# Optimization experiments

Hardware: AMD Instinct MI355X
Metric: run time of the kernel (lower is better)

## Reference

```python
import jax, jax.numpy as jnp
import numpy as np

B, S, D = 4, 2048, 1024
H, DK, DV, DFF = 16, 64, 64, 4096
EPS = 1e-5


def layer_norm(x, g, b):
    mu = jnp.mean(x, axis=-1, keepdims=True)
    var = jnp.mean((x - mu) ** 2, axis=-1, keepdims=True)
    return (x - mu) * jax.lax.rsqrt(var + EPS) * g + b


def setup_inputs() -> dict:
    key = jax.random.key(0)
    ks = jax.random.split(key, 12)
    s = lambda fan_in: 1.0 / np.sqrt(fan_in)
    return {
        "x": jax.random.normal(ks[0], (B, S, D), dtype=jnp.float32),
        # per-head projections stacked: [H, D, DK/DV] (x @ W layout)
        "Wq": jax.random.normal(ks[1], (H, D, DK), dtype=jnp.float32) * s(D),
        "Wk": jax.random.normal(ks[2], (H, D, DK), dtype=jnp.float32) * s(D),
        "Wv": jax.random.normal(ks[3], (H, D, DV), dtype=jnp.float32) * s(D),
        "Wo": jax.random.normal(ks[4], (H * DV, D), dtype=jnp.float32) * s(H * DV),
        "ln1_g": jnp.ones((D,), dtype=jnp.float32),
        "ln1_b": jnp.zeros((D,), dtype=jnp.float32),
        "W1": jax.random.normal(ks[5], (D, DFF), dtype=jnp.float32) * s(D),
        "b1": jnp.zeros((DFF,), dtype=jnp.float32),
        "W2": jax.random.normal(ks[6], (DFF, D), dtype=jnp.float32) * s(DFF),
        "b2": jnp.zeros((D,), dtype=jnp.float32),
        "ln2_g": jnp.ones((D,), dtype=jnp.float32),
        "ln2_b": jnp.zeros((D,), dtype=jnp.float32),
    }


def reference(x, Wq, Wk, Wv, Wo, ln1_g, ln1_b, W1, b1, W2, b2, ln2_g, ln2_b):
    # --- multi-head causal self-attention (all heads vectorized) ---
    q = jnp.einsum("bsd,hdk->bhsk", x, Wq)
    k = jnp.einsum("bsd,hdk->bhsk", x, Wk)
    v = jnp.einsum("bsd,hdv->bhsv", x, Wv)
    # NOTE: original scales by 1/sqrt(x.shape[-1]) == 1/sqrt(d_model)
    scale = 1.0 / np.sqrt(D).astype(np.float32)
    scores = jnp.einsum("bhsk,bhtk->bhst", q, k) * scale  # [B,H,S,S]
    causal = jnp.tril(jnp.ones((S, S), dtype=bool))
    scores = jnp.where(causal, scores, -jnp.inf)
    attn = jax.nn.softmax(scores, axis=-1)
    ctx = jnp.einsum("bhst,bhtv->bhsv", attn, v)  # [B,H,S,DV]
    # concat heads (head-major last dim, matches torch.cat order)
    ctx = ctx.transpose(0, 2, 1, 3).reshape(B, S, H * DV)
    attn_out = ctx @ Wo  # [B,S,D]
    # Sublayer 1 (dropout is identity in eval)
    h1 = layer_norm(x + attn_out, ln1_g, ln1_b)
    # --- FFN ---
    ff = jax.nn.relu(h1 @ W1 + b1) @ W2 + b2
    # Sublayer 2
    return layer_norm(h1 + ff, ln2_g, ln2_b)
```

## Files before the change

kernel.cpp:

```cpp
#include <hip/hip_runtime.h>

#define DEV __device__ __forceinline__

using f16x8 = _Float16 __attribute__((ext_vector_type(8)));
using f16x4 = _Float16 __attribute__((ext_vector_type(4)));
using f32x4 = float __attribute__((ext_vector_type(4)));

DEV f32x4 mfma16(f16x8 a, f16x8 b, f32x4 c) {
    return __builtin_amdgcn_mfma_f32_16x16x32_f16(a, b, c, 0, 0, 0);
}

DEV void gload16(const void* g, void* l) {
    __builtin_amdgcn_global_load_lds(
        (const __attribute__((address_space(1))) void*)g,
        (__attribute__((address_space(3))) void*)l, 16, 0, 0);
}

template <int MODE>
__global__ __launch_bounds__(256, 2) void gemm_bt(
    const _Float16* __restrict__ A, const _Float16* __restrict__ Bt,
    int M, int N, int K,
    const float* __restrict__ ep0, const float* __restrict__ ep1,
    void* __restrict__ o0, void* __restrict__ o1, void* __restrict__ o2)
{
    __shared__ __align__(16) _Float16 As[128 * 64];
    __shared__ __align__(16) _Float16 Bs[128 * 64];
    const int tid  = threadIdx.x;
    const int wave = tid >> 6, lane = tid & 63;
    const int l16  = lane & 15, g = lane >> 4;
    const int m0 = blockIdx.x * 128, n0 = blockIdx.y * 128;
    const int wm = (wave >> 1) * 64, wn = (wave & 1) * 64;

    f32x4 acc[4][4] = {};

    for (int kt = 0; kt < K; kt += 64) {
#pragma unroll
        for (int it = 0; it < 4; ++it) {
            const int off  = it * 4096 + tid * 16;
            const int row  = off >> 7;
            const int colb = (off & 127) ^ ((row & 7) << 4);
            gload16(A + (size_t)(m0 + row) * K + kt + (colb >> 1), (char*)As + off);
        }
#pragma unroll
        for (int it = 0; it < 4; ++it) {
            const int off  = it * 4096 + tid * 16;
            const int row  = off >> 7;
            const int colb = (off & 127) ^ ((row & 7) << 4);
            gload16(Bt + (size_t)(n0 + row) * K + kt + (colb >> 1), (char*)Bs + off);
        }
        __syncthreads();
#pragma unroll
        for (int kk = 0; kk < 2; ++kk) {
            f16x8 af[4], bfv[4];
#pragma unroll
            for (int i = 0; i < 4; ++i) {
                const int ar = wm + i * 16 + l16;
                const int cb = ((kk * 32 + g * 8) << 1) ^ ((ar & 7) << 4);
                af[i] = *(const f16x8*)((const char*)As + (ar << 7) + cb);
            }
#pragma unroll
            for (int j = 0; j < 4; ++j) {
                const int br = wn + j * 16 + l16;
                const int cb = ((kk * 32 + g * 8) << 1) ^ ((br & 7) << 4);
                bfv[j] = *(const f16x8*)((const char*)Bs + (br << 7) + cb);
            }
#pragma unroll
            for (int i = 0; i < 4; ++i)
#pragma unroll
                for (int j = 0; j < 4; ++j)
                    acc[i][j] = mfma16(af[i], bfv[j], acc[i][j]);
        }
        __syncthreads();
    }

#pragma unroll
    for (int i = 0; i < 4; ++i) {
#pragma unroll
        for (int j = 0; j < 4; ++j) {
#pragma unroll
            for (int r = 0; r < 4; ++r) {
                const int m = m0 + wm + i * 16 + g * 4 + r;
                const int n = n0 + wn + j * 16 + l16;
                const float val = acc[i][j][r];
                if constexpr (MODE == 0) {
                    const int b = m >> 11, s = m & 2047;
                    const int which = n >> 10, hh = (n >> 6) & 15, dd = n & 63;
                    const size_t bh = (size_t)(b * 16 + hh);
                    if (which == 0) {
                        ((_Float16*)o0)[(bh * 2048 + s) * 64 + dd] =
                            (_Float16)(val * 0.04508422f);
                    } else if (which == 1) {
                        ((_Float16*)o1)[(bh * 2048 + s) * 64 + dd] = (_Float16)val;
                    } else {
                        ((_Float16*)o2)[(bh * 64 + dd) * 2048 + s] = (_Float16)val;
                    }
                } else if constexpr (MODE == 1) {
                    const size_t idx = (size_t)m * N + n;
                    ((float*)o0)[idx] = val + ep0[idx];
                } else if constexpr (MODE == 2) {
                    float v = val + ep0[n];
                    ((_Float16*)o0)[(size_t)m * N + n] = (_Float16)(v > 0.f ? v : 0.f);
                } else {
                    const size_t idx = (size_t)m * N + n;
                    ((float*)o0)[idx] = val + ep0[n] + ep1[idx];
                }
            }
        }
    }
}

DEV void stage_kv(const _Float16* __restrict__ Kh, const _Float16* __restrict__ Vh,
                  int kb0, char* ksb, char* vsb, int tid)
{
#pragma unroll
    for (int it = 0; it < 2; ++it) {
        const int off  = it * 4096 + tid * 16;
        const int row  = off >> 7;
        const int colb = (off & 127) ^ ((row & 7) << 4);
        gload16(Kh + (size_t)(kb0 + row) * 64 + (colb >> 1), ksb + off);
    }
#pragma unroll
    for (int it = 0; it < 2; ++it) {
        const int off  = it * 4096 + tid * 16;
        const int row  = off >> 7;
        const int colb = (off & 127) ^ ((row & 7) << 4);
        gload16(Vh + (size_t)row * 2048 + kb0 + (colb >> 1), vsb + off);
    }
}

__global__ __launch_bounds__(256, 4) void attn_kernel(
    const _Float16* __restrict__ Q, const _Float16* __restrict__ Kb,
    const _Float16* __restrict__ Vt, _Float16* __restrict__ ctx)
{
    __shared__ __align__(16) char smem[40960];
    const int tid = threadIdx.x;
    const int w = tid >> 6, lane = tid & 63;
    const int l16 = lane & 15, g = lane >> 4;
    const int lid = blockIdx.x + (blockIdx.y << 4);
    const int bh  = (lid & 7) * 8 + (lid >> 7);
    const int tA  = (lid >> 3) & 15;
    const int b = bh >> 4, h = bh & 15;

    const _Float16* Kh = Kb + (size_t)bh * 2048 * 64;
    const _Float16* Vh = Vt + (size_t)bh * 64 * 2048;
    const int swl = (l16 & 7) << 4;
    char* prow = smem + 32768 + w * 2048 + l16 * 128;

    for (int half = 0; half < 2; ++half) {
        const int T = half ? (31 - tA) : tA;
        const int qbase = T * 64 + w * 16;
        const int qg = qbase + l16;
        const int nt = T + 1;

        const _Float16* qrow = Q + ((size_t)bh * 2048 + qg) * 64;
        const f16x8 qf0 = *(const f16x8*)(qrow + g * 8);
        const f16x8 qf1 = *(const f16x8*)(qrow + 32 + g * 8);

        f32x4 cacc[4] = {};
        float l_run = 0.f;

        stage_kv(Kh, Vh, 0, smem, smem + 16384, tid);
        if (nt > 1) stage_kv(Kh, Vh, 64, smem + 8192, smem + 24576, tid);

        for (int kt = 0; kt < nt; ++kt) {
            const int bufo = (kt & 1) << 13;
            char* kbuf = smem + bufo;
            char* vbuf = smem + 16384 + bufo;

            if (kt + 1 < nt) asm volatile("s_waitcnt vmcnt(4)" ::: "memory");
            else             asm volatile("s_waitcnt vmcnt(0)" ::: "memory");
            __builtin_amdgcn_s_barrier();
            __builtin_amdgcn_sched_barrier(0);

            f32x4 st[4];
            __builtin_amdgcn_s_setprio(1);
#pragma unroll
            for (int s = 0; s < 4; ++s) {
                const char* kr = kbuf + (16 * s + l16) * 128;
                const f16x8 klo = *(const f16x8*)(kr + ((g * 16) ^ swl));
                const f16x8 khi = *(const f16x8*)(kr + ((64 + g * 16) ^ swl));
                f32x4 a0 = {0.f, 0.f, 0.f, 0.f};
                a0 = mfma16(klo, qf0, a0);
                st[s] = mfma16(khi, qf1, a0);
            }
            __builtin_amdgcn_s_setprio(0);

            if (kt == nt - 1) {
#pragma unroll
                for (int s = 0; s < 4; ++s)
#pragma unroll
                    for (int r = 0; r < 4; ++r) {
                        const int kg = kt * 64 + s * 16 + g * 4 + r;
                        if (kg > qg) st[s][r] = -INFINITY;
                    }
            }

            float tsum = 0.f;
#pragma unroll
            for (int s = 0; s < 4; ++s) {
                f16x4 p;
#pragma unroll
                for (int r = 0; r < 4; ++r) {
                    const float e = __builtin_amdgcn_exp2f(st[s][r]);
                    tsum += e;
                    p[r] = (_Float16)e;
                }
                *(f16x4*)(prow + ((s * 32 + g * 8) ^ swl)) = p;
            }
            tsum += __shfl_xor(tsum, 16);
            tsum += __shfl_xor(tsum, 32);
            l_run += tsum;

            const f16x8 pf0 = *(const f16x8*)(prow + ((g * 16) ^ swl));
            const f16x8 pf1 = *(const f16x8*)(prow + ((64 + g * 16) ^ swl));
            __builtin_amdgcn_s_setprio(1);
#pragma unroll
            for (int jt = 0; jt < 4; ++jt) {
                const char* vr = vbuf + (jt * 16 + l16) * 128;
                const f16x8 vlo = *(const f16x8*)(vr + ((g * 16) ^ swl));
                const f16x8 vhi = *(const f16x8*)(vr + ((64 + g * 16) ^ swl));
                cacc[jt] = mfma16(pf0, vlo, cacc[jt]);
                cacc[jt] = mfma16(pf1, vhi, cacc[jt]);
            }
            __builtin_amdgcn_s_setprio(0);

            __builtin_amdgcn_sched_barrier(0);
            __builtin_amdgcn_s_barrier();
            if (kt + 2 < nt)
                stage_kv(Kh, Vh, (kt + 2) * 64, kbuf, vbuf, tid);
        }

        __builtin_amdgcn_s_barrier();

        const float inv = 1.f / l_run;
        f32x4 il;
#pragma unroll
        for (int r = 0; r < 4; ++r) il[r] = __shfl(inv, g * 4 + r);
#pragma unroll
        for (int jt = 0; jt < 4; ++jt)
#pragma unroll
            for (int r = 0; r < 4; ++r)
                ctx[((size_t)b * 2048 + qbase + g * 4 + r) * 1024 + h * 64 + jt * 16 + l16]
                    = (_Float16)(cacc[jt][r] * il[r]);
    }
}

__global__ __launch_bounds__(256) void ln_kernel(
    const float* __restrict__ in, const float* __restrict__ gam, const float* __restrict__ bet,
    float* __restrict__ out32, _Float16* __restrict__ out16)
{
    const int row = blockIdx.x, tid = threadIdx.x;
    const float4 x = ((const float4*)(in + (size_t)row * 1024))[tid];
    float s  = x.x + x.y + x.z + x.w;
    float s2 = x.x * x.x + x.y * x.y + x.z * x.z + x.w * x.w;
#pragma unroll
    for (int o = 32; o > 0; o >>= 1) {
        s  += __shfl_xor(s, o);
        s2 += __shfl_xor(s2, o);
    }
    __shared__ float red[8];
    if ((tid & 63) == 0) { red[tid >> 6] = s; red[4 + (tid >> 6)] = s2; }
    __syncthreads();
    const float S  = red[0] + red[1] + red[2] + red[3];
    const float S2 = red[4] + red[5] + red[6] + red[7];
    const float mu = S * (1.f / 1024.f);
    const float ir = rsqrtf(S2 * (1.f / 1024.f) - mu * mu + 1e-5f);
    const float4 gv = ((const float4*)gam)[tid];
    const float4 bv = ((const float4*)bet)[tid];
    float4 o;
    o.x = (x.x - mu) * ir * gv.x + bv.x;
    o.y = (x.y - mu) * ir * gv.y + bv.y;
    o.z = (x.z - mu) * ir * gv.z + bv.z;
    o.w = (x.w - mu) * ir * gv.w + bv.w;
    if (out32) ((float4*)(out32 + (size_t)row * 1024))[tid] = o;
    if (out16) {
        f16x4 h;
        h[0] = (_Float16)o.x; h[1] = (_Float16)o.y; h[2] = (_Float16)o.z; h[3] = (_Float16)o.w;
        *(f16x4*)(out16 + (size_t)row * 1024 + tid * 4) = h;
    }
}

__global__ __launch_bounds__(256) void cast_f16(const float* __restrict__ in,
                                                _Float16* __restrict__ out, int n4)
{
    const int i = blockIdx.x * 256 + threadIdx.x;
    if (i < n4) {
        const float4 v = ((const float4*)in)[i];
        f16x4 h;
        h[0] = (_Float16)v.x; h[1] = (_Float16)v.y; h[2] = (_Float16)v.z; h[3] = (_Float16)v.w;
        ((f16x4*)out)[i] = h;
    }
}

__global__ __launch_bounds__(256) void transpose_cast(const float* __restrict__ src,
                                                      _Float16* __restrict__ dst, int K, int N)
{
    __shared__ float tile[64][65];
    const int n0 = blockIdx.x * 64, k0 = blockIdx.y * 64;
    const int tid = threadIdx.x;
#pragma unroll
    for (int it = 0; it < 16; ++it) {
        const int idx = it * 256 + tid;
        const int r = idx >> 6, c = idx & 63;
        tile[r][c] = src[(size_t)(k0 + r) * N + n0 + c];
    }
    __syncthreads();
#pragma unroll
    for (int it = 0; it < 16; ++it) {
        const int idx = it * 256 + tid;
        const int r = idx >> 6, c = idx & 63;
        dst[(size_t)(n0 + r) * K + k0 + c] = (_Float16)tile[c][r];
    }
}

__global__ __launch_bounds__(256) void pack_qkv_w(const float* __restrict__ Wq,
                                                  const float* __restrict__ Wk,
                                                  const float* __restrict__ Wv,
                                                  _Float16* __restrict__ dst)
{
    __shared__ float tile[64][65];
    const int n0 = blockIdx.x * 64, d0 = blockIdx.y * 64;
    const int which = n0 >> 10, hh = (n0 >> 6) & 15;
    const float* W = which == 0 ? Wq : (which == 1 ? Wk : Wv);
    const int tid = threadIdx.x;
#pragma unroll
    for (int it = 0; it < 16; ++it) {
        const int idx = it * 256 + tid;
        const int r = idx >> 6, c = idx & 63;
        tile[r][c] = W[((size_t)hh * 1024 + d0 + r) * 64 + c];
    }
    __syncthreads();
#pragma unroll
    for (int it = 0; it < 16; ++it) {
        const int idx = it * 256 + tid;
        const int r = idx >> 6, c = idx & 63;
        dst[(size_t)(n0 + r) * 1024 + d0 + c] = (_Float16)tile[c][r];
    }
}

extern "C" void kernel_launch(void* const* d_in, const int* in_sizes, int n_in,
                              void* d_out, int out_size, void* d_ws, size_t ws_size,
                              hipStream_t stream)
{
    const float* x    = (const float*)d_in[0];
    const float* Wq   = (const float*)d_in[1];
    const float* Wk   = (const float*)d_in[2];
    const float* Wv   = (const float*)d_in[3];
    const float* Wo   = (const float*)d_in[4];
    const float* ln1g = (const float*)d_in[5];
    const float* ln1b = (const float*)d_in[6];
    const float* W1   = (const float*)d_in[7];
    const float* b1   = (const float*)d_in[8];
    const float* W2   = (const float*)d_in[9];
    const float* b2   = (const float*)d_in[10];
    const float* ln2g = (const float*)d_in[11];
    const float* ln2b = (const float*)d_in[12];
    float* out = (float*)d_out;

    char* ws = (char*)d_ws;
    size_t off = 0;
    auto alloc = [&](size_t bytes) {
        void* p = ws + off;
        off += (bytes + 255) & ~(size_t)255;
        return p;
    };
    _Float16* x_h   = (_Float16*)alloc(8192ULL * 1024 * 2);
    _Float16* wqkv  = (_Float16*)alloc(3072ULL * 1024 * 2);
    _Float16* wo_t  = (_Float16*)alloc(1024ULL * 1024 * 2);
    _Float16* w1_t  = (_Float16*)alloc(4096ULL * 1024 * 2);
    _Float16* w2_t  = (_Float16*)alloc(1024ULL * 4096 * 2);
    _Float16* qbuf  = (_Float16*)alloc(8192ULL * 1024 * 2);
    _Float16* kbuf  = (_Float16*)alloc(8192ULL * 1024 * 2);
    _Float16* vt    = (_Float16*)alloc(8192ULL * 1024 * 2);
    _Float16* ctx   = (_Float16*)alloc(8192ULL * 1024 * 2);
    _Float16* ff1   = qbuf;
    float*    resid = (float*)alloc(8192ULL * 1024 * 4);
    float*    h1f   = (float*)alloc(8192ULL * 1024 * 4);
    _Float16* h1h   = (_Float16*)alloc(8192ULL * 1024 * 2);
    if (off > ws_size) return;

    cast_f16<<<8192, 256, 0, stream>>>(x, x_h, 2097152);
    pack_qkv_w<<<dim3(48, 16), 256, 0, stream>>>(Wq, Wk, Wv, wqkv);
    transpose_cast<<<dim3(16, 16), 256, 0, stream>>>(Wo, wo_t, 1024, 1024);
    transpose_cast<<<dim3(64, 16), 256, 0, stream>>>(W1, w1_t, 1024, 4096);
    transpose_cast<<<dim3(16, 64), 256, 0, stream>>>(W2, w2_t, 4096, 1024);

    gemm_bt<0><<<dim3(64, 24), 256, 0, stream>>>(x_h, wqkv, 8192, 3072, 1024,
                                                 nullptr, nullptr, qbuf, kbuf, vt);
    attn_kernel<<<dim3(16, 64), 256, 0, stream>>>(qbuf, kbuf, vt, ctx);
    gemm_bt<1><<<dim3(64, 8), 256, 0, stream>>>(ctx, wo_t, 8192, 1024, 1024,
                                                x, nullptr, resid, nullptr, nullptr);
    ln_kernel<<<8192, 256, 0, stream>>>(resid, ln1g, ln1b, h1f, h1h);
    gemm_bt<2><<<dim3(64, 32), 256, 0, stream>>>(h1h, w1_t, 8192, 4096, 1024,
                                                 b1, nullptr, ff1, nullptr, nullptr);
    gemm_bt<3><<<dim3(64, 8), 256, 0, stream>>>(ff1, w2_t, 8192, 1024, 4096,
                                                b2, h1f, resid, nullptr, nullptr);
    ln_kernel<<<8192, 256, 0, stream>>>(resid, ln2g, ln2b, out, nullptr);
}
```

Baseline: 365.4 us.

## Store residual streams in fp16 and vectorize weight transpose kernels

```diff
diff --git a/kernel.cpp b/kernel.cpp
--- a/kernel.cpp
+++ b/kernel.cpp
@@ -20,7 +20,7 @@
 __global__ __launch_bounds__(256, 2) void gemm_bt(
     const _Float16* __restrict__ A, const _Float16* __restrict__ Bt,
     int M, int N, int K,
-    const float* __restrict__ ep0, const float* __restrict__ ep1,
+    const float* __restrict__ ep0, const _Float16* __restrict__ eph,
     void* __restrict__ o0, void* __restrict__ o1, void* __restrict__ o2)
 {
     __shared__ __align__(16) _Float16 As[128 * 64];
@@ -96,13 +96,13 @@
                     }
                 } else if constexpr (MODE == 1) {
                     const size_t idx = (size_t)m * N + n;
-                    ((float*)o0)[idx] = val + ep0[idx];
+                    ((_Float16*)o0)[idx] = (_Float16)(val + (float)eph[idx]);
                 } else if constexpr (MODE == 2) {
                     float v = val + ep0[n];
                     ((_Float16*)o0)[(size_t)m * N + n] = (_Float16)(v > 0.f ? v : 0.f);
                 } else {
                     const size_t idx = (size_t)m * N + n;
-                    ((float*)o0)[idx] = val + ep0[n] + ep1[idx];
+                    ((_Float16*)o0)[idx] = (_Float16)(val + ep0[n] + (float)eph[idx]);
                 }
             }
         }
@@ -246,11 +246,13 @@
 }
 
 __global__ __launch_bounds__(256) void ln_kernel(
-    const float* __restrict__ in, const float* __restrict__ gam, const float* __restrict__ bet,
+    const _Float16* __restrict__ in, const float* __restrict__ gam,
+    const float* __restrict__ bet,
     float* __restrict__ out32, _Float16* __restrict__ out16)
 {
     const int row = blockIdx.x, tid = threadIdx.x;
-    const float4 x = ((const float4*)(in + (size_t)row * 1024))[tid];
+    const f16x4 xh = *(const f16x4*)(in + (size_t)row * 1024 + tid * 4);
+    float4 x = {(float)xh[0], (float)xh[1], (float)xh[2], (float)xh[3]};
     float s  = x.x + x.y + x.z + x.w;
     float s2 = x.x * x.x + x.y * x.y + x.z * x.z + x.w * x.w;
 #pragma unroll
@@ -295,21 +297,25 @@
 __global__ __launch_bounds__(256) void transpose_cast(const float* __restrict__ src,
                                                       _Float16* __restrict__ dst, int K, int N)
 {
-    __shared__ float tile[64][65];
+    __shared__ float tile[64][68];
     const int n0 = blockIdx.x * 64, k0 = blockIdx.y * 64;
     const int tid = threadIdx.x;
-#pragma unroll
-    for (int it = 0; it < 16; ++it) {
-        const int idx = it * 256 + tid;
-        const int r = idx >> 6, c = idx & 63;
-        tile[r][c] = src[(size_t)(k0 + r) * N + n0 + c];
+    const int rr = tid >> 4, cc = (tid & 15) * 4;
+#pragma unroll
+    for (int it = 0; it < 4; ++it) {
+        const int r = it * 16 + rr;
+        const float4 v = *(const float4*)&src[(size_t)(k0 + r) * N + n0 + cc];
+        tile[r][cc] = v.x; tile[r][cc + 1] = v.y;
+        tile[r][cc + 2] = v.z; tile[r][cc + 3] = v.w;
     }
     __syncthreads();
 #pragma unroll
-    for (int it = 0; it < 16; ++it) {
-        const int idx = it * 256 + tid;
-        const int r = idx >> 6, c = idx & 63;
-        dst[(size_t)(n0 + r) * K + k0 + c] = (_Float16)tile[c][r];
+    for (int it = 0; it < 4; ++it) {
+        const int n = it * 16 + rr;
+        f16x4 h;
+        h[0] = (_Float16)tile[cc + 0][n]; h[1] = (_Float16)tile[cc + 1][n];
+        h[2] = (_Float16)tile[cc + 2][n]; h[3] = (_Float16)tile[cc + 3][n];
+        *(f16x4*)&dst[(size_t)(n0 + n) * K + k0 + cc] = h;
     }
 }
 
@@ -318,23 +324,27 @@
                                                   const float* __restrict__ Wv,
                                                   _Float16* __restrict__ dst)
 {
-    __shared__ float tile[64][65];
+    __shared__ float tile[64][68];
     const int n0 = blockIdx.x * 64, d0 = blockIdx.y * 64;
     const int which = n0 >> 10, hh = (n0 >> 6) & 15;
     const float* W = which == 0 ? Wq : (which == 1 ? Wk : Wv);
     const int tid = threadIdx.x;
-#pragma unroll
-    for (int it = 0; it < 16; ++it) {
-        const int idx = it * 256 + tid;
-        const int r = idx >> 6, c = idx & 63;
-        tile[r][c] = W[((size_t)hh * 1024 + d0 + r) * 64 + c];
+    const int rr = tid >> 4, cc = (tid & 15) * 4;
+#pragma unroll
+    for (int it = 0; it < 4; ++it) {
+        const int r = it * 16 + rr;
+        const float4 v = *(const float4*)&W[((size_t)hh * 1024 + d0 + r) * 64 + cc];
+        tile[r][cc] = v.x; tile[r][cc + 1] = v.y;
+        tile[r][cc + 2] = v.z; tile[r][cc + 3] = v.w;
     }
     __syncthreads();
 #pragma unroll
-    for (int it = 0; it < 16; ++it) {
-        const int idx = it * 256 + tid;
-        const int r = idx >> 6, c = idx & 63;
-        dst[(size_t)(n0 + r) * 1024 + d0 + c] = (_Float16)tile[c][r];
+    for (int it = 0; it < 4; ++it) {
+        const int kk = it * 16 + rr;
+        f16x4 h;
+        h[0] = (_Float16)tile[cc + 0][kk]; h[1] = (_Float16)tile[cc + 1][kk];
+        h[2] = (_Float16)tile[cc + 2][kk]; h[3] = (_Float16)tile[cc + 3][kk];
+        *(f16x4*)&dst[(size_t)(n0 + kk) * 1024 + d0 + cc] = h;
     }
 }
 
@@ -364,19 +374,18 @@
         off += (bytes + 255) & ~(size_t)255;
         return p;
     };
-    _Float16* x_h   = (_Float16*)alloc(8192ULL * 1024 * 2);
-    _Float16* wqkv  = (_Float16*)alloc(3072ULL * 1024 * 2);
-    _Float16* wo_t  = (_Float16*)alloc(1024ULL * 1024 * 2);
-    _Float16* w1_t  = (_Float16*)alloc(4096ULL * 1024 * 2);
-    _Float16* w2_t  = (_Float16*)alloc(1024ULL * 4096 * 2);
-    _Float16* qbuf  = (_Float16*)alloc(8192ULL * 1024 * 2);
-    _Float16* kbuf  = (_Float16*)alloc(8192ULL * 1024 * 2);
-    _Float16* vt    = (_Float16*)alloc(8192ULL * 1024 * 2);
-    _Float16* ctx   = (_Float16*)alloc(8192ULL * 1024 * 2);
-    _Float16* ff1   = qbuf;
-    float*    resid = (float*)alloc(8192ULL * 1024 * 4);
-    float*    h1f   = (float*)alloc(8192ULL * 1024 * 4);
-    _Float16* h1h   = (_Float16*)alloc(8192ULL * 1024 * 2);
+    _Float16* x_h    = (_Float16*)alloc(8192ULL * 1024 * 2);
+    _Float16* wqkv   = (_Float16*)alloc(3072ULL * 1024 * 2);
+    _Float16* wo_t   = (_Float16*)alloc(1024ULL * 1024 * 2);
+    _Float16* w1_t   = (_Float16*)alloc(4096ULL * 1024 * 2);
+    _Float16* w2_t   = (_Float16*)alloc(1024ULL * 4096 * 2);
+    _Float16* qbuf   = (_Float16*)alloc(8192ULL * 1024 * 2);
+    _Float16* kbuf   = (_Float16*)alloc(8192ULL * 1024 * 2);
+    _Float16* vt     = (_Float16*)alloc(8192ULL * 1024 * 2);
+    _Float16* ctx    = (_Float16*)alloc(8192ULL * 1024 * 2);
+    _Float16* ff1    = qbuf;
+    _Float16* residh = (_Float16*)alloc(8192ULL * 1024 * 2);
+    _Float16* h1h    = (_Float16*)alloc(8192ULL * 1024 * 2);
     if (off > ws_size) return;
 
     cast_f16<<<8192, 256, 0, stream>>>(x, x_h, 2097152);
@@ -389,11 +398,11 @@
                                                  nullptr, nullptr, qbuf, kbuf, vt);
     attn_kernel<<<dim3(16, 64), 256, 0, stream>>>(qbuf, kbuf, vt, ctx);
     gemm_bt<1><<<dim3(64, 8), 256, 0, stream>>>(ctx, wo_t, 8192, 1024, 1024,
-                                                x, nullptr, resid, nullptr, nullptr);
-    ln_kernel<<<8192, 256, 0, stream>>>(resid, ln1g, ln1b, h1f, h1h);
+                                                nullptr, x_h, residh, nullptr, nullptr);
+    ln_kernel<<<8192, 256, 0, stream>>>(residh, ln1g, ln1b, nullptr, h1h);
     gemm_bt<2><<<dim3(64, 32), 256, 0, stream>>>(h1h, w1_t, 8192, 4096, 1024,
                                                  b1, nullptr, ff1, nullptr, nullptr);
     gemm_bt<3><<<dim3(64, 8), 256, 0, stream>>>(ff1, w2_t, 8192, 1024, 4096,
-                                                b2, h1f, resid, nullptr, nullptr);
-    ln_kernel<<<8192, 256, 0, stream>>>(resid, ln2g, ln2b, out, nullptr);
-}
+                                                b2, h1h, residh, nullptr, nullptr);
+    ln_kernel<<<8192, 256, 0, stream>>>(residh, ln2g, ln2b, out, nullptr);
+}
```

Result: faster. 349.9 us (-4.3%).
